# Performance work log

Hardware: AMD Instinct MI355X
Metric: run time of the kernel (lower is better)

## Reference

```python
import jax, jax.numpy as jnp
import numpy as np

N_NODES = 50000
N_EDGES = 400000


def setup_inputs() -> dict:
    key = jax.random.key(0)
    ks = jax.random.split(key, 8)
    d_in, d_hid, d_out = 512, 512, 256
    feats = jax.random.normal(ks[0], (N_NODES, d_in), dtype=jnp.float32)
    src = jax.random.randint(ks[1], (N_EDGES,), 0, N_NODES, dtype=jnp.int32)
    dst = jax.random.randint(ks[2], (N_EDGES,), 0, N_NODES, dtype=jnp.int32)
    # Glorot-ish scaled weights so activations stay O(1)
    W0 = jax.random.normal(ks[3], (d_in, d_hid), dtype=jnp.float32) / np.sqrt(d_in)
    b0 = jnp.zeros((d_hid,), jnp.float32)
    W1 = jax.random.normal(ks[4], (d_hid, d_hid), dtype=jnp.float32) / np.sqrt(d_hid)
    b1 = jnp.zeros((d_hid,), jnp.float32)
    W2 = jax.random.normal(ks[5], (d_hid, d_out), dtype=jnp.float32) / np.sqrt(d_hid)
    b2 = jnp.zeros((d_out,), jnp.float32)
    return {"feats": feats, "src": src, "dst": dst,
            "W0": W0, "b0": b0, "W1": W1, "b1": b1, "W2": W2, "b2": b2}


def _sage_conv_gcn(h, src, dst, W, b, deg):
    # DGL SAGEConv aggregator_type='gcn':
    # h_neigh[v] = (sum_{u->v} h[u] + h[v]) / (in_deg(v) + 1); out = h_neigh @ W + b
    agg = jax.ops.segment_sum(h[src], dst, num_segments=h.shape[0])  # [N, d]
    h_neigh = (agg + h) / (deg[:, None] + 1.0)
    return h_neigh @ W + b


def reference(feats, src, dst, W0, b0, W1, b1, W2, b2):
    N = feats.shape[0]
    deg = jax.ops.segment_sum(jnp.ones((src.shape[0],), feats.dtype), dst,
                              num_segments=N)  # in-degree per node
    h = jax.nn.relu(_sage_conv_gcn(feats, src, dst, W0, b0, deg))  # dropout p=0, norm none
    h = jax.nn.relu(_sage_conv_gcn(h, src, dst, W1, b1, deg))
    h = _sage_conv_gcn(h, src, dst, W2, b2, deg)  # final layer: no activation
    return h
```

## Files before the change

kernel.cpp:

```cpp
#include <hip/hip_runtime.h>
#include <stdint.h>

#define N_NODES 50000
#define N_EDGES 400000
#define MPAD    50048
#define SCAN_B  49

typedef __bf16 bf16x8 __attribute__((ext_vector_type(8)));
typedef float  f32x4  __attribute__((ext_vector_type(4)));
typedef unsigned short ushort_t;
typedef unsigned int   uint_t;

__device__ __forceinline__ ushort_t f2b(float f){
    uint_t x = __float_as_uint(f);
    x += 0x7FFFu + ((x >> 16) & 1u);
    return (ushort_t)(x >> 16);
}
__device__ __forceinline__ float b2f(ushort_t h){
    return __uint_as_float(((uint_t)h) << 16);
}

__global__ void zero_two(int* a, int* b, int n){
    int i = blockIdx.x * blockDim.x + threadIdx.x;
    if (i < n){ a[i] = 0; b[i] = 0; }
}

__global__ void hist_kernel(const int* __restrict__ dst, int* __restrict__ deg, int E){
    int i = blockIdx.x * blockDim.x + threadIdx.x;
    if (i < E) atomicAdd(&deg[dst[i]], 1);
}

__global__ __launch_bounds__(1024) void blk_scan_kernel(
        const int* __restrict__ deg, int* __restrict__ offs,
        int* __restrict__ bsum, int n){
    __shared__ int buf[1024];
    const int t = threadIdx.x, b = blockIdx.x;
    const int i = b * 1024 + t;
    int v = (i < n) ? deg[i] : 0;
    buf[t] = v; __syncthreads();
    for (int off = 1; off < 1024; off <<= 1){
        int x = (t >= off) ? buf[t - off] : 0;
        __syncthreads();
        buf[t] += x;
        __syncthreads();
    }
    if (i < n) offs[i] = buf[t] - v;
    if (t == 1023) bsum[b] = buf[1023];
}

__global__ void bsum_scan_kernel(int* __restrict__ bsum, int nb){
    int t = threadIdx.x;
    int orig = (t < nb) ? bsum[t] : 0;
    int v = orig;
    #pragma unroll
    for (int off = 1; off < 64; off <<= 1){
        int x = __shfl_up(v, off, 64);
        if (t >= off) v += x;
    }
    if (t < nb) bsum[t] = v - orig;
}

__global__ __launch_bounds__(1024) void add_off_kernel(
        int* __restrict__ offs, const int* __restrict__ bsum, int n){
    int i = blockIdx.x * 1024 + threadIdx.x;
    if (i < n) offs[i] += bsum[blockIdx.x];
    if (i == 0) offs[n] = N_EDGES;
}

__global__ void fill_kernel(const int* __restrict__ src, const int* __restrict__ dst,
                            const int* __restrict__ offs, int* __restrict__ cursor,
                            int* __restrict__ nbr, int E){
    int i = blockIdx.x * blockDim.x + threadIdx.x;
    if (i < E){
        int d = dst[i];
        int p = atomicAdd(&cursor[d], 1);
        nbr[offs[d] + p] = src[i];
    }
}

__global__ void f2b_kernel(const float4* __restrict__ in, ushort4* __restrict__ out, int n4){
    int i = blockIdx.x * blockDim.x + threadIdx.x;
    if (i < n4){
        float4 v = in[i];
        ushort4 o; o.x = f2b(v.x); o.y = f2b(v.y); o.z = f2b(v.z); o.w = f2b(v.w);
        out[i] = o;
    }
}

__global__ void wtrans_kernel(const float* __restrict__ W, ushort_t* __restrict__ Wt,
                              int K, int N){
    int i = blockIdx.x * blockDim.x + threadIdx.x;
    if (i < K * N){
        int n = i / K, k = i - n * K;
        Wt[i] = f2b(W[k * N + n]);
    }
}

__device__ __forceinline__ void load16(const void* g, void* l){
    __builtin_amdgcn_global_load_lds((const __attribute__((address_space(1))) void*)g,
                                     (__attribute__((address_space(3))) void*)l, 16, 0, 0);
}

__global__ __launch_bounds__(256, 2) void gemm_bt(const ushort_t* __restrict__ A,
                                                  const ushort_t* __restrict__ Bt,
                                                  ushort_t* __restrict__ C,
                                                  int N, int K){
    __shared__ ushort_t As[128 * 32];
    __shared__ ushort_t Bs[256 * 32];
    const int tid  = threadIdx.x, lane = tid & 63, wave = tid >> 6;
    const int bm = blockIdx.x, bn = blockIdx.y;
    const int fr = lane & 15;
    const int fk = (lane >> 4) * 8;
    const int wm = (wave >> 1) * 64, wn = (wave & 1) * 128;
    f32x4 acc[4][8] = {};

    for (int kt = 0; kt < K; kt += 32){
        __syncthreads();
        #pragma unroll
        for (int i = 0; i < 2; i++){
            int s = tid + i * 256;
            load16(A + (size_t)(bm * 128 + (s >> 2)) * K + kt + (s & 3) * 8,
                   (char*)As + s * 16);
        }
        #pragma unroll
        for (int i = 0; i < 4; i++){
            int s = tid + i * 256;
            load16(Bt + (size_t)(bn * 256 + (s >> 2)) * K + kt + (s & 3) * 8,
                   (char*)Bs + s * 16);
        }
        __syncthreads();
        bf16x8 af[4], bf[8];
        #pragma unroll
        for (int t = 0; t < 4; t++)
            af[t] = *(const bf16x8*)(const void*)(As + (wm + t * 16 + fr) * 32 + fk);
        #pragma unroll
        for (int t = 0; t < 8; t++)
            bf[t] = *(const bf16x8*)(const void*)(Bs + (wn + t * 16 + fr) * 32 + fk);
        #pragma unroll
        for (int tm = 0; tm < 4; tm++)
            #pragma unroll
            for (int tn = 0; tn < 8; tn++)
                acc[tm][tn] = __builtin_amdgcn_mfma_f32_16x16x32_bf16(
                                  af[tm], bf[tn], acc[tm][tn], 0, 0, 0);
    }
    const int r0 = (lane >> 4) * 4, c0 = lane & 15;
    #pragma unroll
    for (int tm = 0; tm < 4; tm++){
        #pragma unroll
        for (int tn = 0; tn < 8; tn++){
            int rbase = bm * 128 + wm + tm * 16 + r0;
            int cidx  = bn * 256 + wn + tn * 16 + c0;
            #pragma unroll
            for (int reg = 0; reg < 4; reg++)
                C[(size_t)(rbase + reg) * N + cidx] = f2b(acc[tm][tn][reg]);
        }
    }
}

__device__ __forceinline__ void acc8(float* a, uint4 y){
    a[0] += b2f((ushort_t)(y.x & 0xffff)); a[1] += b2f((ushort_t)(y.x >> 16));
    a[2] += b2f((ushort_t)(y.y & 0xffff)); a[3] += b2f((ushort_t)(y.y >> 16));
    a[4] += b2f((ushort_t)(y.z & 0xffff)); a[5] += b2f((ushort_t)(y.z >> 16));
    a[6] += b2f((ushort_t)(y.w & 0xffff)); a[7] += b2f((ushort_t)(y.w >> 16));
}
__device__ __forceinline__ void acc4(float* a, uint2 y){
    a[0] += b2f((ushort_t)(y.x & 0xffff)); a[1] += b2f((ushort_t)(y.x >> 16));
    a[2] += b2f((ushort_t)(y.y & 0xffff)); a[3] += b2f((ushort_t)(y.y >> 16));
}

__global__ __launch_bounds__(256) void agg_relu_kernel(
        const ushort_t* __restrict__ Y, const int* __restrict__ offs,
        const int* __restrict__ nbr, const float* __restrict__ bias,
        ushort_t* __restrict__ H){
    const int lane = threadIdx.x & 63, wave = threadIdx.x >> 6;
    const int v = blockIdx.x * 4 + wave;
    const int off = lane * 8;
    float a[8];
    {   uint4 y = *(const uint4*)(const void*)(Y + (size_t)v * 512 + off);
        a[0] = b2f((ushort_t)(y.x & 0xffff)); a[1] = b2f((ushort_t)(y.x >> 16));
        a[2] = b2f((ushort_t)(y.y & 0xffff)); a[3] = b2f((ushort_t)(y.y >> 16));
        a[4] = b2f((ushort_t)(y.z & 0xffff)); a[5] = b2f((ushort_t)(y.z >> 16));
        a[6] = b2f((ushort_t)(y.w & 0xffff)); a[7] = b2f((ushort_t)(y.w >> 16)); }
    const int beg = offs[v], end = offs[v + 1];
    int i = beg;
    for (; i + 8 <= end; i += 8){
        uint4 yy[8];
        #pragma unroll
        for (int j = 0; j < 8; j++){
            int u = nbr[i + j];
            yy[j] = *(const uint4*)(const void*)(Y + (size_t)u * 512 + off);
        }
        #pragma unroll
        for (int j = 0; j < 8; j++) acc8(a, yy[j]);
    }
    for (; i + 4 <= end; i += 4){
        uint4 yy[4];
        #pragma unroll
        for (int j = 0; j < 4; j++){
            int u = nbr[i + j];
            yy[j] = *(const uint4*)(const void*)(Y + (size_t)u * 512 + off);
        }
        #pragma unroll
        for (int j = 0; j < 4; j++) acc8(a, yy[j]);
    }
    for (; i < end; i++){
        int u = nbr[i];
        uint4 y = *(const uint4*)(const void*)(Y + (size_t)u * 512 + off);
        acc8(a, y);
    }
    const float inv = 1.0f / (float)(end - beg + 1);
    float4 bb0 = ((const float4*)bias)[lane * 2];
    float4 bb1 = ((const float4*)bias)[lane * 2 + 1];
    float r[8];
    r[0] = a[0]*inv + bb0.x; r[1] = a[1]*inv + bb0.y;
    r[2] = a[2]*inv + bb0.z; r[3] = a[3]*inv + bb0.w;
    r[4] = a[4]*inv + bb1.x; r[5] = a[5]*inv + bb1.y;
    r[6] = a[6]*inv + bb1.z; r[7] = a[7]*inv + bb1.w;
    #pragma unroll
    for (int j = 0; j < 8; j++) r[j] = r[j] > 0.f ? r[j] : 0.f;
    uint4 o;
    o.x = (uint_t)f2b(r[0]) | ((uint_t)f2b(r[1]) << 16);
    o.y = (uint_t)f2b(r[2]) | ((uint_t)f2b(r[3]) << 16);
    o.z = (uint_t)f2b(r[4]) | ((uint_t)f2b(r[5]) << 16);
    o.w = (uint_t)f2b(r[6]) | ((uint_t)f2b(r[7]) << 16);
    *(uint4*)(void*)(H + (size_t)v * 512 + off) = o;
}

__global__ __launch_bounds__(256) void agg_out_kernel(
        const ushort_t* __restrict__ Y, const int* __restrict__ offs,
        const int* __restrict__ nbr, const float* __restrict__ bias,
        float* __restrict__ out){
    const int lane = threadIdx.x & 63, wave = threadIdx.x >> 6;
    const int v = blockIdx.x * 4 + wave;
    const int off = lane * 4;
    float a[4];
    {   uint2 y = *(const uint2*)(const void*)(Y + (size_t)v * 256 + off);
        a[0] = b2f((ushort_t)(y.x & 0xffff)); a[1] = b2f((ushort_t)(y.x >> 16));
        a[2] = b2f((ushort_t)(y.y & 0xffff)); a[3] = b2f((ushort_t)(y.y >> 16)); }
    const int beg = offs[v], end = offs[v + 1];
    int i = beg;
    for (; i + 8 <= end; i += 8){
        uint2 yy[8];
        #pragma unroll
        for (int j = 0; j < 8; j++){
            int u = nbr[i + j];
            yy[j] = *(const uint2*)(const void*)(Y + (size_t)u * 256 + off);
        }
        #pragma unroll
        for (int j = 0; j < 8; j++) acc4(a, yy[j]);
    }
    for (; i + 4 <= end; i += 4){
        uint2 yy[4];
        #pragma unroll
        for (int j = 0; j < 4; j++){
            int u = nbr[i + j];
            yy[j] = *(const uint2*)(const void*)(Y + (size_t)u * 256 + off);
        }
        #pragma unroll
        for (int j = 0; j < 4; j++) acc4(a, yy[j]);
    }
    for (; i < end; i++){
        int u = nbr[i];
        uint2 y = *(const uint2*)(const void*)(Y + (size_t)u * 256 + off);
        acc4(a, y);
    }
    const float inv = 1.0f / (float)(end - beg + 1);
    float4 bb = ((const float4*)bias)[lane];
    float4 r;
    r.x = a[0]*inv + bb.x; r.y = a[1]*inv + bb.y;
    r.z = a[2]*inv + bb.z; r.w = a[3]*inv + bb.w;
    ((float4*)out)[v * 64 + lane] = r;
}

extern "C" void kernel_launch(void* const* d_in, const int* in_sizes, int n_in,
                              void* d_out, int out_size, void* d_ws, size_t ws_size,
                              hipStream_t stream) {
    const float* feats = (const float*)d_in[0];
    const int*   src   = (const int*)  d_in[1];
    const int*   dst   = (const int*)  d_in[2];
    const float* W0    = (const float*)d_in[3];
    const float* b0    = (const float*)d_in[4];
    const float* W1    = (const float*)d_in[5];
    const float* b1    = (const float*)d_in[6];
    const float* W2    = (const float*)d_in[7];
    const float* b2    = (const float*)d_in[8];
    float* out = (float*)d_out;

    char* w = (char*)d_ws;
    ushort_t* Abuf = (ushort_t*)w;  w += (size_t)MPAD * 512 * 2;
    ushort_t* Ybuf = (ushort_t*)w;  w += (size_t)MPAD * 512 * 2;
    ushort_t* W0t  = (ushort_t*)w;  w += 512 * 512 * 2;
    ushort_t* W1t  = (ushort_t*)w;  w += 512 * 512 * 2;
    ushort_t* W2t  = (ushort_t*)w;  w += 256 * 512 * 2;
    int* deg    = (int*)w;          w += 50048 * 4;
    int* offs   = (int*)w;          w += 50056 * 4;
    int* cursor = (int*)w;          w += 50048 * 4;
    int* nbr    = (int*)w;          w += (size_t)N_EDGES * 4;
    int* bsum   = (int*)w;          w += 64 * 4;

    zero_two<<<(N_NODES + 255) / 256, 256, 0, stream>>>(deg, cursor, N_NODES);
    hist_kernel<<<(N_EDGES + 255) / 256, 256, 0, stream>>>(dst, deg, N_EDGES);
    blk_scan_kernel<<<SCAN_B, 1024, 0, stream>>>(deg, offs, bsum, N_NODES);
    bsum_scan_kernel<<<1, 64, 0, stream>>>(bsum, SCAN_B);
    add_off_kernel<<<SCAN_B, 1024, 0, stream>>>(offs, bsum, N_NODES);
    fill_kernel<<<(N_EDGES + 255) / 256, 256, 0, stream>>>(src, dst, offs, cursor, nbr, N_EDGES);

    int n4 = N_NODES * 512 / 4;
    f2b_kernel<<<(n4 + 255) / 256, 256, 0, stream>>>((const float4*)feats, (ushort4*)Abuf, n4);
    wtrans_kernel<<<(512 * 512 + 255) / 256, 256, 0, stream>>>(W0, W0t, 512, 512);
    wtrans_kernel<<<(512 * 512 + 255) / 256, 256, 0, stream>>>(W1, W1t, 512, 512);
    wtrans_kernel<<<(512 * 256 + 255) / 256, 256, 0, stream>>>(W2, W2t, 512, 256);

    dim3 g01(MPAD / 128, 512 / 256);
    dim3 g2 (MPAD / 128, 256 / 256);

    gemm_bt<<<g01, 256, 0, stream>>>(Abuf, W0t, Ybuf, 512, 512);
    agg_relu_kernel<<<N_NODES / 4, 256, 0, stream>>>(Ybuf, offs, nbr, b0, Abuf);
    gemm_bt<<<g01, 256, 0, stream>>>(Abuf, W1t, Ybuf, 512, 512);
    agg_relu_kernel<<<N_NODES / 4, 256, 0, stream>>>(Ybuf, offs, nbr, b1, Abuf);
    gemm_bt<<<g2, 256, 0, stream>>>(Abuf, W2t, Ybuf, 256, 512);
    agg_out_kernel<<<N_NODES / 4, 256, 0, stream>>>(Ybuf, offs, nbr, b2, out);
}
```

Measured before the change: 518.6 us.

## Split aggregation into column slices with edge-parallel lanes and shuffle reduction

The aggregation kernels now give each wave one node and one 64-column slice. The 8 lane groups each handle every 8th neighbour (the self row is folded in as the first entry) and combine partial sums with xor shuffles. This raises parallelism for low-degree nodes and removes the serial per-lane neighbour loop. The cost is more blocks, repeated reads of offs and nbr per slice, and shuffle overhead. The GEMM is also split into three identically bodied per-layer kernels, which likely only helps profiling.

```diff
diff --git a/kernel.cpp b/kernel.cpp
--- a/kernel.cpp
+++ b/kernel.cpp
@@ -101,10 +101,10 @@
                                      (__attribute__((address_space(3))) void*)l, 16, 0, 0);
 }
 
-__global__ __launch_bounds__(256, 2) void gemm_bt(const ushort_t* __restrict__ A,
-                                                  const ushort_t* __restrict__ Bt,
-                                                  ushort_t* __restrict__ C,
-                                                  int N, int K){
+__device__ __forceinline__ void gemm_body(const ushort_t* __restrict__ A,
+                                          const ushort_t* __restrict__ Bt,
+                                          ushort_t* __restrict__ C,
+                                          int N, int K){
     __shared__ ushort_t As[128 * 32];
     __shared__ ushort_t Bs[256 * 32];
     const int tid  = threadIdx.x, lane = tid & 63, wave = tid >> 6;
@@ -157,73 +157,64 @@
     }
 }
 
+__global__ __launch_bounds__(256, 2) void gemm_l0(const ushort_t* __restrict__ A,
+        const ushort_t* __restrict__ Bt, ushort_t* __restrict__ C, int N, int K){
+    gemm_body(A, Bt, C, N, K);
+}
+__global__ __launch_bounds__(256, 2) void gemm_l1(const ushort_t* __restrict__ A,
+        const ushort_t* __restrict__ Bt, ushort_t* __restrict__ C, int N, int K){
+    gemm_body(A, Bt, C, N, K);
+}
+__global__ __launch_bounds__(256, 2) void gemm_l2(const ushort_t* __restrict__ A,
+        const ushort_t* __restrict__ Bt, ushort_t* __restrict__ C, int N, int K){
+    gemm_body(A, Bt, C, N, K);
+}
+
 __device__ __forceinline__ void acc8(float* a, uint4 y){
     a[0] += b2f((ushort_t)(y.x & 0xffff)); a[1] += b2f((ushort_t)(y.x >> 16));
     a[2] += b2f((ushort_t)(y.y & 0xffff)); a[3] += b2f((ushort_t)(y.y >> 16));
     a[4] += b2f((ushort_t)(y.z & 0xffff)); a[5] += b2f((ushort_t)(y.z >> 16));
     a[6] += b2f((ushort_t)(y.w & 0xffff)); a[7] += b2f((ushort_t)(y.w >> 16));
 }
-__device__ __forceinline__ void acc4(float* a, uint2 y){
-    a[0] += b2f((ushort_t)(y.x & 0xffff)); a[1] += b2f((ushort_t)(y.x >> 16));
-    a[2] += b2f((ushort_t)(y.y & 0xffff)); a[3] += b2f((ushort_t)(y.y >> 16));
-}
 
 __global__ __launch_bounds__(256) void agg_relu_kernel(
         const ushort_t* __restrict__ Y, const int* __restrict__ offs,
         const int* __restrict__ nbr, const float* __restrict__ bias,
         ushort_t* __restrict__ H){
     const int lane = threadIdx.x & 63, wave = threadIdx.x >> 6;
-    const int v = blockIdx.x * 4 + wave;
-    const int off = lane * 8;
-    float a[8];
-    {   uint4 y = *(const uint4*)(const void*)(Y + (size_t)v * 512 + off);
-        a[0] = b2f((ushort_t)(y.x & 0xffff)); a[1] = b2f((ushort_t)(y.x >> 16));
-        a[2] = b2f((ushort_t)(y.y & 0xffff)); a[3] = b2f((ushort_t)(y.y >> 16));
-        a[4] = b2f((ushort_t)(y.z & 0xffff)); a[5] = b2f((ushort_t)(y.z >> 16));
-        a[6] = b2f((ushort_t)(y.w & 0xffff)); a[7] = b2f((ushort_t)(y.w >> 16)); }
+    const int s = blockIdx.x & 7;
+    const int v = (blockIdx.x >> 3) * 4 + wave;
+    const int grp = lane >> 3, sub = lane & 7;
+    const int col = s * 64 + sub * 8;
+    float a[8] = {0.f,0.f,0.f,0.f,0.f,0.f,0.f,0.f};
     const int beg = offs[v], end = offs[v + 1];
-    int i = beg;
-    for (; i + 8 <= end; i += 8){
-        uint4 yy[8];
-        #pragma unroll
-        for (int j = 0; j < 8; j++){
-            int u = nbr[i + j];
-            yy[j] = *(const uint4*)(const void*)(Y + (size_t)u * 512 + off);
-        }
-        #pragma unroll
-        for (int j = 0; j < 8; j++) acc8(a, yy[j]);
-    }
-    for (; i + 4 <= end; i += 4){
-        uint4 yy[4];
-        #pragma unroll
-        for (int j = 0; j < 4; j++){
-            int u = nbr[i + j];
-            yy[j] = *(const uint4*)(const void*)(Y + (size_t)u * 512 + off);
-        }
-        #pragma unroll
-        for (int j = 0; j < 4; j++) acc8(a, yy[j]);
-    }
-    for (; i < end; i++){
-        int u = nbr[i];
-        uint4 y = *(const uint4*)(const void*)(Y + (size_t)u * 512 + off);
+    for (int i = beg - 1 + grp; i < end; i += 8){
+        int u = (i < beg) ? v : nbr[i];
+        uint4 y = *(const uint4*)(const void*)(Y + (size_t)u * 512 + col);
         acc8(a, y);
     }
-    const float inv = 1.0f / (float)(end - beg + 1);
-    float4 bb0 = ((const float4*)bias)[lane * 2];
-    float4 bb1 = ((const float4*)bias)[lane * 2 + 1];
-    float r[8];
-    r[0] = a[0]*inv + bb0.x; r[1] = a[1]*inv + bb0.y;
-    r[2] = a[2]*inv + bb0.z; r[3] = a[3]*inv + bb0.w;
-    r[4] = a[4]*inv + bb1.x; r[5] = a[5]*inv + bb1.y;
-    r[6] = a[6]*inv + bb1.z; r[7] = a[7]*inv + bb1.w;
     #pragma unroll
-    for (int j = 0; j < 8; j++) r[j] = r[j] > 0.f ? r[j] : 0.f;
-    uint4 o;
-    o.x = (uint_t)f2b(r[0]) | ((uint_t)f2b(r[1]) << 16);
-    o.y = (uint_t)f2b(r[2]) | ((uint_t)f2b(r[3]) << 16);
-    o.z = (uint_t)f2b(r[4]) | ((uint_t)f2b(r[5]) << 16);
-    o.w = (uint_t)f2b(r[6]) | ((uint_t)f2b(r[7]) << 16);
-    *(uint4*)(void*)(H + (size_t)v * 512 + off) = o;
+    for (int m = 8; m < 64; m <<= 1){
+        #pragma unroll
+        for (int j = 0; j < 8; j++)
+            a[j] += __shfl_xor(a[j], m, 64);
+    }
+    if (grp == 0){
+        const float inv = 1.0f / (float)(end - beg + 1);
+        float4 b0 = *(const float4*)(bias + col);
+        float4 b1 = *(const float4*)(bias + col + 4);
+        float r[8];
+        r[0]=a[0]*inv+b0.x; r[1]=a[1]*inv+b0.y; r[2]=a[2]*inv+b0.z; r[3]=a[3]*inv+b0.w;
+        r[4]=a[4]*inv+b1.x; r[5]=a[5]*inv+b1.y; r[6]=a[6]*inv+b1.z; r[7]=a[7]*inv+b1.w;
+        #pragma unroll
+        for (int j = 0; j < 8; j++) r[j] = r[j] > 0.f ? r[j] : 0.f;
+        uint4 o;
+        o.x = (uint_t)f2b(r[0]) | ((uint_t)f2b(r[1]) << 16);
+        o.y = (uint_t)f2b(r[2]) | ((uint_t)f2b(r[3]) << 16);
+        o.z = (uint_t)f2b(r[4]) | ((uint_t)f2b(r[5]) << 16);
+        o.w = (uint_t)f2b(r[6]) | ((uint_t)f2b(r[7]) << 16);
+        *(uint4*)(void*)(H + (size_t)v * 512 + col) = o;
+    }
 }
 
 __global__ __launch_bounds__(256) void agg_out_kernel(
@@ -231,45 +222,33 @@
         const int* __restrict__ nbr, const float* __restrict__ bias,
         float* __restrict__ out){
     const int lane = threadIdx.x & 63, wave = threadIdx.x >> 6;
-    const int v = blockIdx.x * 4 + wave;
-    const int off = lane * 4;
-    float a[4];
-    {   uint2 y = *(const uint2*)(const void*)(Y + (size_t)v * 256 + off);
-        a[0] = b2f((ushort_t)(y.x & 0xffff)); a[1] = b2f((ushort_t)(y.x >> 16));
-        a[2] = b2f((ushort_t)(y.y & 0xffff)); a[3] = b2f((ushort_t)(y.y >> 16)); }
+    const int s = blockIdx.x & 3;
+    const int v = (blockIdx.x >> 2) * 4 + wave;
+    const int grp = lane >> 3, sub = lane & 7;
+    const int col = s * 64 + sub * 8;
+    float a[8] = {0.f,0.f,0.f,0.f,0.f,0.f,0.f,0.f};
     const int beg = offs[v], end = offs[v + 1];
-    int i = beg;
-    for (; i + 8 <= end; i += 8){
-        uint2 yy[8];
-        #pragma unroll
-        for (int j = 0; j < 8; j++){
-            int u = nbr[i + j];
-            yy[j] = *(const uint2*)(const void*)(Y + (size_t)u * 256 + off);
-        }
-        #pragma unroll
-        for (int j = 0; j < 8; j++) acc4(a, yy[j]);
-    }
-    for (; i + 4 <= end; i += 4){
-        uint2 yy[4];
-        #pragma unroll
-        for (int j = 0; j < 4; j++){
-            int u = nbr[i + j];
-            yy[j] = *(const uint2*)(const void*)(Y + (size_t)u * 256 + off);
-        }
-        #pragma unroll
-        for (int j = 0; j < 4; j++) acc4(a, yy[j]);
-    }
-    for (; i < end; i++){
-        int u = nbr[i];
-        uint2 y = *(const uint2*)(const void*)(Y + (size_t)u * 256 + off);
-        acc4(a, y);
-    }
-    const float inv = 1.0f / (float)(end - beg + 1);
-    float4 bb = ((const float4*)bias)[lane];
-    float4 r;
-    r.x = a[0]*inv + bb.x; r.y = a[1]*inv + bb.y;
-    r.z = a[2]*inv + bb.z; r.w = a[3]*inv + bb.w;
-    ((float4*)out)[v * 64 + lane] = r;
+    for (int i = beg - 1 + grp; i < end; i += 8){
+        int u = (i < beg) ? v : nbr[i];
+        uint4 y = *(const uint4*)(const void*)(Y + (size_t)u * 256 + col);
+        acc8(a, y);
+    }
+    #pragma unroll
+    for (int m = 8; m < 64; m <<= 1){
+        #pragma unroll
+        for (int j = 0; j < 8; j++)
+            a[j] += __shfl_xor(a[j], m, 64);
+    }
+    if (grp == 0){
+        const float inv = 1.0f / (float)(end - beg + 1);
+        float4 b0 = *(const float4*)(bias + col);
+        float4 b1 = *(const float4*)(bias + col + 4);
+        float4 r0, r1;
+        r0.x=a[0]*inv+b0.x; r0.y=a[1]*inv+b0.y; r0.z=a[2]*inv+b0.z; r0.w=a[3]*inv+b0.w;
+        r1.x=a[4]*inv+b1.x; r1.y=a[5]*inv+b1.y; r1.z=a[6]*inv+b1.z; r1.w=a[7]*inv+b1.w;
+        *(float4*)(out + (size_t)v * 256 + col)     = r0;
+        *(float4*)(out + (size_t)v * 256 + col + 4) = r1;
+    }
 }
 
 extern "C" void kernel_launch(void* const* d_in, const int* in_sizes, int n_in,
@@ -314,10 +293,10 @@
     dim3 g01(MPAD / 128, 512 / 256);
     dim3 g2 (MPAD / 128, 256 / 256);
 
-    gemm_bt<<<g01, 256, 0, stream>>>(Abuf, W0t, Ybuf, 512, 512);
-    agg_relu_kernel<<<N_NODES / 4, 256, 0, stream>>>(Ybuf, offs, nbr, b0, Abuf);
-    gemm_bt<<<g01, 256, 0, stream>>>(Abuf, W1t, Ybuf, 512, 512);
-    agg_relu_kernel<<<N_NODES / 4, 256, 0, stream>>>(Ybuf, offs, nbr, b1, Abuf);
-    gemm_bt<<<g2, 256, 0, stream>>>(Abuf, W2t, Ybuf, 256, 512);
-    agg_out_kernel<<<N_NODES / 4, 256, 0, stream>>>(Ybuf, offs, nbr, b2, out);
-}
+    gemm_l0<<<g01, 256, 0, stream>>>(Abuf, W0t, Ybuf, 512, 512);
+    agg_relu_kernel<<<(N_NODES / 4) * 8, 256, 0, stream>>>(Ybuf, offs, nbr, b0, Abuf);
+    gemm_l1<<<g01, 256, 0, stream>>>(Abuf, W1t, Ybuf, 512, 512);
+    agg_relu_kernel<<<(N_NODES / 4) * 8, 256, 0, stream>>>(Ybuf, offs, nbr, b1, Abuf);
+    gemm_l2<<<g2, 256, 0, stream>>>(Abuf, W2t, Ybuf, 256, 512);
+    agg_out_kernel<<<(N_NODES / 4) * 4, 256, 0, stream>>>(Ybuf, offs, nbr, b2, out);
+}
```

Measured after the change: 681.9 us. +31.5%, slower.
